# Performance work log

Hardware: AMD Instinct MI355X
Metric: run time of the kernel (lower is better)

## Reference

```python
import jax, jax.numpy as jnp
import numpy as np

B = 1024
IN_Q = 2048
IN_KV = 2048
NH = 16
D = 64
INNER = NH * D
TF = 4
NC = 2
EPS = 1e-5
SLOPE = 0.01  # LeakyReLU default negative slope


def setup_inputs() -> dict:
    key = jax.random.key(0)
    ks = jax.random.split(key, 8)
    s = 0.02
    return {
        "q_input": jax.random.normal(ks[0], (B, IN_Q), jnp.float32),
        "kv_input": jax.random.normal(ks[1], (B, IN_KV), jnp.float32),
        "Wq": jax.random.normal(ks[2], (INNER, IN_Q), jnp.float32) * s,
        "bq": jax.random.normal(ks[3], (INNER,), jnp.float32) * s,
        "Wkv": jax.random.normal(ks[4], (2 * INNER, IN_KV), jnp.float32) * s,
        "bkv": jax.random.normal(ks[5], (2 * INNER,), jnp.float32) * s,
        "bn_w": jnp.ones((TF,), jnp.float32),
        "bn_b": jnp.zeros((TF,), jnp.float32),
        "Wo": jax.random.normal(ks[6], (NC, TF), jnp.float32) * s,
        "bo": jax.random.normal(ks[7], (NC,), jnp.float32) * s,
    }


def reference(q_input, kv_input, Wq, bq, Wkv, bkv, bn_w, bn_b, Wo, bo):
    b = q_input.shape[0]
    # projections: [B, NH, D] and [B, NH, 2D]
    q = (q_input @ Wq.T + bq).reshape(b, NH, D)
    kv = (kv_input @ Wkv.T + bkv).reshape(b, NH, 2 * D)
    k, v = kv[..., :D], kv[..., D:]
    # sim[b,n] = k[b,n,:] . q[b,n,:]  (per-head scalar score)
    sim = jnp.einsum("bnd,bnd->bn", k, q)
    att = jax.nn.softmax(sim, axis=-1)  # softmax over heads
    # torch.matmul([B,NH], [B,NH,D]) broadcast -> out[i,j,:] = sum_n att[j,n] v[i,n,:]
    att_out = jnp.einsum("jn,ind->ijd", att, v)  # [B, B, D]
    flat = att_out.reshape(b, b * D)  # [B, B*D]
    # AdaptiveAvgPool1d to TF bins (L % TF == 0 -> exact reshape-mean)
    pooled = flat.reshape(b, TF, (b * D) // TF).mean(axis=-1)  # [B, TF]
    x = jnp.where(pooled >= 0, pooled, SLOPE * pooled)  # LeakyReLU
    # BatchNorm1d, train mode (batch stats, biased variance)
    mean = x.mean(axis=0)
    var = x.var(axis=0)
    x = (x - mean) * jax.lax.rsqrt(var + EPS) * bn_w + bn_b
    # dropout(p=0.0) is identity
    return x @ Wo.T + bo  # [B, NC]
```

## Files before the change

kernel.cpp:

```cpp
#include <hip/hip_runtime.h>
#include <hip/hip_bf16.h>

#define EPS 1e-5f
#define SLOPE 0.01f

typedef __attribute__((ext_vector_type(8))) short bfrag8;
typedef __attribute__((ext_vector_type(4))) float f32x4;

#define AS1 __attribute__((address_space(1)))
#define AS3 __attribute__((address_space(3)))

#define WS_SIM_OFF   0u
#define WS_S_OFF     65536u
#define WS_WVS_OFF   131072u
#define WS_BVS_OFF   262144u
#define WS_AIMG_OFF  262208u
#define WS_BIMG_OFF  8650816u

__device__ __forceinline__ unsigned short f2bf(float f) {
    union { float f; unsigned int u; } x; x.f = f;
    unsigned int r = (x.u + 0x7FFFu + ((x.u >> 16) & 1u)) >> 16;
    return (unsigned short)r;
}
__device__ __forceinline__ uint4 pack8(const float4& a, const float4& b) {
    uint4 r;
    r.x = (unsigned)f2bf(a.x) | ((unsigned)f2bf(a.y) << 16);
    r.y = (unsigned)f2bf(a.z) | ((unsigned)f2bf(a.w) << 16);
    r.z = (unsigned)f2bf(b.x) | ((unsigned)f2bf(b.y) << 16);
    r.w = (unsigned)f2bf(b.z) | ((unsigned)f2bf(b.w) << 16);
    return r;
}

#define PREP_A    524288
#define PREP_B2   (PREP_A + 524288)
#define PREP_WVSE (PREP_B2 + 32768)
#define PREP_SIMZ (PREP_WVSE + 16384)
#define PREP_END  (PREP_SIMZ + 16)

__global__ __launch_bounds__(256) void prep_kernel(
        const float* __restrict__ qin, const float* __restrict__ kvin,
        const float* __restrict__ Wq, const float* __restrict__ Wkv,
        const float* __restrict__ bkv, unsigned char* __restrict__ ws) {
    int gid = blockIdx.x * 256 + threadIdx.x;
    if (gid < PREP_A) {
        int p  = gid & 511;
        int kt = (gid >> 9) & 31;
        int mt = (gid >> 14) & 15;
        int s2 = gid >> 18;
        int rit = p >> 3;
        int gk = (p & 7) ^ (rit & 7);
        int row = mt * 64 + rit;
        int k = kt * 64 + gk * 8;
        const float* src = (s2 ? kvin : qin) + (size_t)row * 2048 + k;
        float4 v0 = *(const float4*)src;
        float4 v1 = *(const float4*)(src + 4);
        *(uint4*)(ws + WS_AIMG_OFF + (size_t)gid * 16) = pack8(v0, v1);
    } else if (gid < PREP_B2) {
        int g2 = gid - PREP_A;
        int p  = g2 & 511;
        int kt = (g2 >> 9) & 31;
        int dh = (g2 >> 14) & 1;
        int h  = g2 >> 15;
        int cit = p >> 3;
        int gk = (p & 7) ^ (cit & 7);
        int k = kt * 64 + gk * 8;
        const float* wrow;
        if (cit < 32) wrow = Wq  + (size_t)(h * 64 + dh * 32 + cit) * 2048;
        else          wrow = Wkv + (size_t)(h * 128 + dh * 32 + (cit - 32)) * 2048;
        float4 v0 = *(const float4*)(wrow + k);
        float4 v1 = *(const float4*)(wrow + k + 4);
        *(uint4*)(ws + WS_BIMG_OFF + (size_t)g2 * 16) = pack8(v0, v1);
    } else if (gid < PREP_WVSE) {
        int g2 = gid - PREP_B2;
        int n = g2 >> 11, c = g2 & 2047;
        const float* base = Wkv + (size_t)(n * 128 + 64) * 2048 + c;
        float s = 0.f;
        #pragma unroll 8
        for (int d = 0; d < 64; ++d) s += base[(size_t)d * 2048];
        ((float*)(ws + WS_WVS_OFF))[c * 16 + n] = s;
    } else if (gid < PREP_SIMZ) {
        ((float*)(ws + WS_SIM_OFF))[gid - PREP_WVSE] = 0.f;
    } else if (gid < PREP_END) {
        int n = gid - PREP_SIMZ;
        float b = 0.f;
        #pragma unroll
        for (int d = 0; d < 64; ++d) b += bkv[n * 128 + 64 + d];
        ((float*)(ws + WS_BVS_OFF))[n] = b;
    }
}

__global__ __launch_bounds__(256, 2) void gemm_sim_kernel(unsigned char* __restrict__ ws,
        const float* __restrict__ bq, const float* __restrict__ bkv) {
    __shared__ alignas(16) unsigned short LAq[3][4096];
    __shared__ alignas(16) unsigned short LAkv[3][4096];
    __shared__ alignas(16) unsigned short LB[3][4096];

    const int t = threadIdx.x;
    const int w = t >> 6, l = t & 63;
    const int hd = blockIdx.x, mt = blockIdx.y;
    const int h = hd >> 1, dh = hd & 1;
    const int qk = w >> 1, wr = w & 1;
    const int lrow = l & 15, lhi = l >> 4;
    const int m0 = mt * 64;

    const unsigned char* aqBase = ws + WS_AIMG_OFF + (size_t)mt * 262144u;
    const unsigned char* akBase = aqBase + 4194304u;
    const unsigned char* bBase  = ws + WS_BIMG_OFF + (size_t)hd * 262144u;
    float* sim = (float*)(ws + WS_SIM_OFF);

    int offA[2][2], offB[2][2];
    #pragma unroll
    for (int ks = 0; ks < 2; ++ks)
        #pragma unroll
        for (int i = 0; i < 2; ++i) {
            int r = wr * 32 + i * 16 + lrow;
            int c = qk * 32 + i * 16 + lrow;
            offA[ks][i] = r * 128 + (((ks * 4 + lhi) ^ (r & 7)) << 4);
            offB[ks][i] = c * 128 + (((ks * 4 + lhi) ^ (c & 7)) << 4);
        }

    f32x4 acc00 = (f32x4)0.f, acc01 = (f32x4)0.f, acc10 = (f32x4)0.f, acc11 = (f32x4)0.f;

#define STAGE(kt_, buf_) do {                                                        \
    const unsigned char* _aq = aqBase + (size_t)(kt_) * 8192;                        \
    const unsigned char* _ak = akBase + (size_t)(kt_) * 8192;                        \
    const unsigned char* _b  = bBase  + (size_t)(kt_) * 8192;                        \
    unsigned char* _dq = ((unsigned char*)&LAq[0][0])  + (size_t)(buf_) * 8192;      \
    unsigned char* _dk = ((unsigned char*)&LAkv[0][0]) + (size_t)(buf_) * 8192;      \
    unsigned char* _db = ((unsigned char*)&LB[0][0])   + (size_t)(buf_) * 8192;      \
    _Pragma("unroll")                                                                \
    for (int _j = 0; _j < 2; ++_j) {                                                 \
        int _p = _j * 256 + t;                                                       \
        __builtin_amdgcn_global_load_lds(                                            \
            (const AS1 unsigned int*)(const void*)(_aq + _p * 16),                   \
            (AS3 unsigned int*)(void*)(_dq + _p * 16), 16, 0, 0);                    \
        __builtin_amdgcn_global_load_lds(                                            \
            (const AS1 unsigned int*)(const void*)(_ak + _p * 16),                   \
            (AS3 unsigned int*)(void*)(_dk + _p * 16), 16, 0, 0);                    \
        __builtin_amdgcn_global_load_lds(                                            \
            (const AS1 unsigned int*)(const void*)(_b + _p * 16),                    \
            (AS3 unsigned int*)(void*)(_db + _p * 16), 16, 0, 0);                    \
    } } while (0)

    STAGE(0, 0);
    STAGE(1, 1);
    asm volatile("s_waitcnt vmcnt(6)" ::: "memory");
    __builtin_amdgcn_sched_barrier(0);
    __builtin_amdgcn_s_barrier();
    __builtin_amdgcn_sched_barrier(0);

    int cur = 0, nxt = 2;
    for (int kt = 0; kt < 32; ++kt) {
        {
            const char* Ab = (const char*)(qk ? &LAkv[0][0] : &LAq[0][0]) + cur * 8192;
            const char* Bb = (const char*)&LB[0][0] + cur * 8192;
            #pragma unroll
            for (int ks = 0; ks < 2; ++ks) {
                bfrag8 fa0 = *(const bfrag8*)(Ab + offA[ks][0]);
                bfrag8 fa1 = *(const bfrag8*)(Ab + offA[ks][1]);
                bfrag8 fb0 = *(const bfrag8*)(Bb + offB[ks][0]);
                bfrag8 fb1 = *(const bfrag8*)(Bb + offB[ks][1]);
                acc00 = __builtin_amdgcn_mfma_f32_16x16x32_bf16(fa0, fb0, acc00, 0, 0, 0);
                acc01 = __builtin_amdgcn_mfma_f32_16x16x32_bf16(fa0, fb1, acc01, 0, 0, 0);
                acc10 = __builtin_amdgcn_mfma_f32_16x16x32_bf16(fa1, fb0, acc10, 0, 0, 0);
                acc11 = __builtin_amdgcn_mfma_f32_16x16x32_bf16(fa1, fb1, acc11, 0, 0, 0);
            }
        }
        if (kt < 30) {
            STAGE(kt + 2, nxt);
            asm volatile("s_waitcnt vmcnt(6)" ::: "memory");
        } else {
            asm volatile("s_waitcnt vmcnt(0)" ::: "memory");
        }
        __builtin_amdgcn_sched_barrier(0);
        __builtin_amdgcn_s_barrier();
        __builtin_amdgcn_sched_barrier(0);
        cur = (cur == 2) ? 0 : cur + 1;
        nxt = (nxt == 2) ? 0 : nxt + 1;
    }
#undef STAGE

    f32x4 acc[2][2] = {{acc00, acc01}, {acc10, acc11}};
    float biasv[2];
    #pragma unroll
    for (int ni = 0; ni < 2; ++ni) {
        int d = dh * 32 + ni * 16 + lrow;
        biasv[ni] = qk ? bkv[h * 128 + d] : bq[h * 64 + d];
    }
    #pragma unroll
    for (int mi = 0; mi < 2; ++mi)
        #pragma unroll
        for (int ni = 0; ni < 2; ++ni)
            #pragma unroll
            for (int r = 0; r < 4; ++r)
                acc[mi][ni][r] += biasv[ni];

    float (*Cq)[32] = (float(*)[32])&LAq[0][0];
    if (!qk) {
        #pragma unroll
        for (int mi = 0; mi < 2; ++mi)
            #pragma unroll
            for (int ni = 0; ni < 2; ++ni)
                #pragma unroll
                for (int r = 0; r < 4; ++r)
                    Cq[wr * 32 + mi * 16 + lhi * 4 + r][ni * 16 + lrow] = acc[mi][ni][r];
    }
    __syncthreads();
    if (qk) {
        #pragma unroll
        for (int mi = 0; mi < 2; ++mi) {
            float pv[4];
            #pragma unroll
            for (int r = 0; r < 4; ++r) {
                int row = wr * 32 + mi * 16 + lhi * 4 + r;
                pv[r] = Cq[row][lrow]      * acc[mi][0][r]
                      + Cq[row][16 + lrow] * acc[mi][1][r];
            }
            #pragma unroll
            for (int r = 0; r < 4; ++r) {
                float v = pv[r];
                v += __shfl_xor(v, 1); v += __shfl_xor(v, 2);
                v += __shfl_xor(v, 4); v += __shfl_xor(v, 8);
                if ((l & 15) == 0) {
                    int row = wr * 32 + mi * 16 + (l >> 4) * 4 + r;
                    atomicAdd(&sim[(m0 + row) * 16 + h], v);
                }
            }
        }
    }
}

__global__ __launch_bounds__(256) void s_kernel(
        const float* __restrict__ kvin, unsigned char* __restrict__ ws) {
    int b = blockIdx.x, t = threadIdx.x;
    int w = t >> 6, l = t & 63;
    __shared__ float SW[4][16];
    int n = t & 15, g = t >> 4;
    const float* kvrow = kvin + (size_t)b * 2048;
    const float* wv = (const float*)(ws + WS_WVS_OFF);
    float p = 0.f;
    #pragma unroll 4
    for (int tt = 0; tt < 128; ++tt) {
        int c = g + (tt << 4);
        p = fmaf(kvrow[c], wv[c * 16 + n], p);
    }
    p += __shfl_xor(p, 16);
    p += __shfl_xor(p, 32);
    if (l < 16) SW[w][n] = p;
    __syncthreads();
    if (t < 16) {
        float sv = SW[0][t] + SW[1][t] + SW[2][t] + SW[3][t]
                 + ((const float*)(ws + WS_BVS_OFF))[t];
        ((float*)(ws + WS_S_OFF))[b * 16 + t] = sv;
    }
}

__global__ __launch_bounds__(1024) void final_kernel(
        const float* __restrict__ bn_w, const float* __restrict__ bn_b,
        const float* __restrict__ Wo, const float* __restrict__ bo,
        const unsigned char* __restrict__ ws, float* __restrict__ out) {
    int t = threadIdx.x;
    int w = t >> 6;
    int l = t & 63;
    __shared__ float Aw[16][16];
    __shared__ float Af[4][16];
    __shared__ float SWs[16][8];
    __shared__ float FS[8];
    __shared__ float sc[4], sh[4];

    float a16[16];
    {
        const float* srow = (const float*)(ws + WS_SIM_OFF) + (size_t)t * 16;
        float4 v0 = *(const float4*)(srow + 0);
        float4 v1 = *(const float4*)(srow + 4);
        float4 v2 = *(const float4*)(srow + 8);
        float4 v3 = *(const float4*)(srow + 12);
        a16[0]=v0.x; a16[1]=v0.y; a16[2]=v0.z; a16[3]=v0.w;
        a16[4]=v1.x; a16[5]=v1.y; a16[6]=v1.z; a16[7]=v1.w;
        a16[8]=v2.x; a16[9]=v2.y; a16[10]=v2.z; a16[11]=v2.w;
        a16[12]=v3.x; a16[13]=v3.y; a16[14]=v3.z; a16[15]=v3.w;
        float m = a16[0];
        #pragma unroll
        for (int n = 1; n < 16; ++n) m = fmaxf(m, a16[n]);
        float den = 0.f;
        #pragma unroll
        for (int n = 0; n < 16; ++n) { a16[n] = expf(a16[n] - m); den += a16[n]; }
        float inv = 1.f / den;
        #pragma unroll
        for (int n = 0; n < 16; ++n) a16[n] *= inv;
    }
    #pragma unroll
    for (int n = 0; n < 16; ++n) {
        float p = a16[n];
        p += __shfl_xor(p, 1);  p += __shfl_xor(p, 2);
        p += __shfl_xor(p, 4);  p += __shfl_xor(p, 8);
        p += __shfl_xor(p, 16); p += __shfl_xor(p, 32);
        a16[n] = p;
    }
    if (l == 0) {
        #pragma unroll
        for (int n = 0; n < 16; ++n) Aw[w][n] = a16[n];
    }
    __syncthreads();
    if (t < 64) {
        int f = t >> 4, n = t & 15;
        Af[f][n] = Aw[4*f][n] + Aw[4*f+1][n] + Aw[4*f+2][n] + Aw[4*f+3][n];
    }
    __syncthreads();

    float sv[16];
    {
        const float* srow = (const float*)(ws + WS_S_OFF) + (size_t)t * 16;
        float4 v0 = *(const float4*)(srow + 0);
        float4 v1 = *(const float4*)(srow + 4);
        float4 v2 = *(const float4*)(srow + 8);
        float4 v3 = *(const float4*)(srow + 12);
        sv[0]=v0.x; sv[1]=v0.y; sv[2]=v0.z; sv[3]=v0.w;
        sv[4]=v1.x; sv[5]=v1.y; sv[6]=v1.z; sv[7]=v1.w;
        sv[8]=v2.x; sv[9]=v2.y; sv[10]=v2.z; sv[11]=v2.w;
        sv[12]=v3.x; sv[13]=v3.y; sv[14]=v3.z; sv[15]=v3.w;
    }
    float x[4];
    #pragma unroll
    for (int f = 0; f < 4; ++f) {
        float p = 0.f;
        #pragma unroll
        for (int n = 0; n < 16; ++n) p = fmaf(Af[f][n], sv[n], p);
        p *= (1.f / 16384.f);
        x[f] = (p >= 0.f) ? p : SLOPE * p;
    }

    float st[8];
    #pragma unroll
    for (int f = 0; f < 4; ++f) { st[f] = x[f]; st[4 + f] = x[f] * x[f]; }
    #pragma unroll
    for (int j = 0; j < 8; ++j) {
        float p = st[j];
        p += __shfl_xor(p, 1);  p += __shfl_xor(p, 2);
        p += __shfl_xor(p, 4);  p += __shfl_xor(p, 8);
        p += __shfl_xor(p, 16); p += __shfl_xor(p, 32);
        st[j] = p;
    }
    if (l == 0) {
        #pragma unroll
        for (int j = 0; j < 8; ++j) SWs[w][j] = st[j];
    }
    __syncthreads();
    if (t < 8) {
        float p = 0.f;
        #pragma unroll
        for (int ww = 0; ww < 16; ++ww) p += SWs[ww][t];
        FS[t] = p;
    }
    __syncthreads();
    if (t < 4) {
        float mean = FS[t] * (1.f / 1024.f);
        float var  = FS[4 + t] * (1.f / 1024.f) - mean * mean;
        float s = bn_w[t] / sqrtf(var + EPS);
        sc[t] = s;
        sh[t] = bn_b[t] - mean * s;
    }
    __syncthreads();

    float o0 = bo[0], o1 = bo[1];
    #pragma unroll
    for (int f = 0; f < 4; ++f) {
        float xh = x[f] * sc[f] + sh[f];
        o0 = fmaf(xh, Wo[f], o0);
        o1 = fmaf(xh, Wo[4 + f], o1);
    }
    *(float2*)(out + (size_t)t * 2) = make_float2(o0, o1);
}

extern "C" void kernel_launch(void* const* d_in, const int* in_sizes, int n_in,
                              void* d_out, int out_size, void* d_ws, size_t ws_size,
                              hipStream_t stream) {
    const float* q_input  = (const float*)d_in[0];
    const float* kv_input = (const float*)d_in[1];
    const float* Wq   = (const float*)d_in[2];
    const float* bq   = (const float*)d_in[3];
    const float* Wkv  = (const float*)d_in[4];
    const float* bkv  = (const float*)d_in[5];
    const float* bn_w = (const float*)d_in[6];
    const float* bn_b = (const float*)d_in[7];
    const float* Wo   = (const float*)d_in[8];
    const float* bo   = (const float*)d_in[9];
    float* out = (float*)d_out;
    unsigned char* ws = (unsigned char*)d_ws;

    hipLaunchKernelGGL(prep_kernel, dim3((PREP_END + 255) / 256), dim3(256), 0, stream,
                       q_input, kv_input, Wq, Wkv, bkv, ws);
    hipLaunchKernelGGL(gemm_sim_kernel, dim3(32, 16), dim3(256), 0, stream,
                       ws, bq, bkv);
    hipLaunchKernelGGL(s_kernel, dim3(1024), dim3(256), 0, stream, kv_input, ws);
    hipLaunchKernelGGL(final_kernel, dim3(1), dim3(1024), 0, stream,
                       bn_w, bn_b, Wo, bo, ws, out);
}
```

Measured before the change: 60.56 us.

## Process two heads per block in sim GEMM to share staged A tiles

The projection/similarity GEMM block now has 512 threads covering two heads (and one half of D) instead of 256 threads covering one head-half. Both heads share the same Q and KV activation tiles staged in LDS, so each activation tile is loaded from global memory once per pair of heads instead of once per head. The grid shrinks to 8x16x2 blocks at one block per CU with a larger LDS footprint. The trade-off is fewer resident blocks per CU, which may reduce latency hiding.

```diff
diff --git a/kernel.cpp b/kernel.cpp
--- a/kernel.cpp
+++ b/kernel.cpp
@@ -89,23 +89,24 @@
     }
 }
 
-__global__ __launch_bounds__(256, 2) void gemm_sim_kernel(unsigned char* __restrict__ ws,
+__global__ __launch_bounds__(512, 1) void gemm_sim_kernel(unsigned char* __restrict__ ws,
         const float* __restrict__ bq, const float* __restrict__ bkv) {
     __shared__ alignas(16) unsigned short LAq[3][4096];
     __shared__ alignas(16) unsigned short LAkv[3][4096];
-    __shared__ alignas(16) unsigned short LB[3][4096];
+    __shared__ alignas(16) unsigned short LB[3][2][4096];
 
     const int t = threadIdx.x;
     const int w = t >> 6, l = t & 63;
-    const int hd = blockIdx.x, mt = blockIdx.y;
-    const int h = hd >> 1, dh = hd & 1;
-    const int qk = w >> 1, wr = w & 1;
+    const int hp = blockIdx.x, mt = blockIdx.y, dh = blockIdx.z;
+    const int qk = w >> 2, hh = (w >> 1) & 1, wr = w & 1;
+    const int h = hp * 2 + hh;
     const int lrow = l & 15, lhi = l >> 4;
     const int m0 = mt * 64;
 
     const unsigned char* aqBase = ws + WS_AIMG_OFF + (size_t)mt * 262144u;
     const unsigned char* akBase = aqBase + 4194304u;
-    const unsigned char* bBase  = ws + WS_BIMG_OFF + (size_t)hd * 262144u;
+    const unsigned char* bBase0 = ws + WS_BIMG_OFF + (size_t)((hp * 2 + 0) * 2 + dh) * 262144u;
+    const unsigned char* bBase1 = ws + WS_BIMG_OFF + (size_t)((hp * 2 + 1) * 2 + dh) * 262144u;
     float* sim = (float*)(ws + WS_SIM_OFF);
 
     int offA[2][2], offB[2][2];
@@ -122,29 +123,27 @@
     f32x4 acc00 = (f32x4)0.f, acc01 = (f32x4)0.f, acc10 = (f32x4)0.f, acc11 = (f32x4)0.f;
 
 #define STAGE(kt_, buf_) do {                                                        \
-    const unsigned char* _aq = aqBase + (size_t)(kt_) * 8192;                        \
-    const unsigned char* _ak = akBase + (size_t)(kt_) * 8192;                        \
-    const unsigned char* _b  = bBase  + (size_t)(kt_) * 8192;                        \
-    unsigned char* _dq = ((unsigned char*)&LAq[0][0])  + (size_t)(buf_) * 8192;      \
-    unsigned char* _dk = ((unsigned char*)&LAkv[0][0]) + (size_t)(buf_) * 8192;      \
-    unsigned char* _db = ((unsigned char*)&LB[0][0])   + (size_t)(buf_) * 8192;      \
-    _Pragma("unroll")                                                                \
-    for (int _j = 0; _j < 2; ++_j) {                                                 \
-        int _p = _j * 256 + t;                                                       \
-        __builtin_amdgcn_global_load_lds(                                            \
-            (const AS1 unsigned int*)(const void*)(_aq + _p * 16),                   \
-            (AS3 unsigned int*)(void*)(_dq + _p * 16), 16, 0, 0);                    \
-        __builtin_amdgcn_global_load_lds(                                            \
-            (const AS1 unsigned int*)(const void*)(_ak + _p * 16),                   \
-            (AS3 unsigned int*)(void*)(_dk + _p * 16), 16, 0, 0);                    \
-        __builtin_amdgcn_global_load_lds(                                            \
-            (const AS1 unsigned int*)(const void*)(_b + _p * 16),                    \
-            (AS3 unsigned int*)(void*)(_db + _p * 16), 16, 0, 0);                    \
-    } } while (0)
+    const unsigned char* _aq = aqBase + (size_t)(kt_) * 8192 + t * 16;               \
+    const unsigned char* _ak = akBase + (size_t)(kt_) * 8192 + t * 16;               \
+    const unsigned char* _b0 = bBase0 + (size_t)(kt_) * 8192 + t * 16;               \
+    const unsigned char* _b1 = bBase1 + (size_t)(kt_) * 8192 + t * 16;               \
+    unsigned char* _dq = ((unsigned char*)&LAq[0][0])  + (size_t)(buf_) * 8192 + t * 16;  \
+    unsigned char* _dk = ((unsigned char*)&LAkv[0][0]) + (size_t)(buf_) * 8192 + t * 16;  \
+    unsigned char* _d0 = ((unsigned char*)&LB[0][0][0]) + (size_t)(buf_) * 16384 + t * 16;        \
+    unsigned char* _d1 = ((unsigned char*)&LB[0][0][0]) + (size_t)(buf_) * 16384 + 8192 + t * 16; \
+    __builtin_amdgcn_global_load_lds((const AS1 unsigned int*)(const void*)_aq,      \
+        (AS3 unsigned int*)(void*)_dq, 16, 0, 0);                                    \
+    __builtin_amdgcn_global_load_lds((const AS1 unsigned int*)(const void*)_ak,      \
+        (AS3 unsigned int*)(void*)_dk, 16, 0, 0);                                    \
+    __builtin_amdgcn_global_load_lds((const AS1 unsigned int*)(const void*)_b0,      \
+        (AS3 unsigned int*)(void*)_d0, 16, 0, 0);                                    \
+    __builtin_amdgcn_global_load_lds((const AS1 unsigned int*)(const void*)_b1,      \
+        (AS3 unsigned int*)(void*)_d1, 16, 0, 0);                                    \
+    } while (0)
 
     STAGE(0, 0);
     STAGE(1, 1);
-    asm volatile("s_waitcnt vmcnt(6)" ::: "memory");
+    asm volatile("s_waitcnt vmcnt(4)" ::: "memory");
     __builtin_amdgcn_sched_barrier(0);
     __builtin_amdgcn_s_barrier();
     __builtin_amdgcn_sched_barrier(0);
@@ -153,7 +152,7 @@
     for (int kt = 0; kt < 32; ++kt) {
         {
             const char* Ab = (const char*)(qk ? &LAkv[0][0] : &LAq[0][0]) + cur * 8192;
-            const char* Bb = (const char*)&LB[0][0] + cur * 8192;
+            const char* Bb = (const char*)&LB[0][0][0] + cur * 16384 + hh * 8192;
             #pragma unroll
             for (int ks = 0; ks < 2; ++ks) {
                 bfrag8 fa0 = *(const bfrag8*)(Ab + offA[ks][0]);
@@ -168,7 +167,7 @@
         }
         if (kt < 30) {
             STAGE(kt + 2, nxt);
-            asm volatile("s_waitcnt vmcnt(6)" ::: "memory");
+            asm volatile("s_waitcnt vmcnt(4)" ::: "memory");
         } else {
             asm volatile("s_waitcnt vmcnt(0)" ::: "memory");
         }
@@ -195,15 +194,17 @@
             for (int r = 0; r < 4; ++r)
                 acc[mi][ni][r] += biasv[ni];
 
-    float (*Cq)[32] = (float(*)[32])&LAq[0][0];
+    float* cqs = (float*)&LAq[0][0];
     if (!qk) {
         #pragma unroll
         for (int mi = 0; mi < 2; ++mi)
             #pragma unroll
             for (int ni = 0; ni < 2; ++ni)
                 #pragma unroll
-                for (int r = 0; r < 4; ++r)
-                    Cq[wr * 32 + mi * 16 + lhi * 4 + r][ni * 16 + lrow] = acc[mi][ni][r];
+                for (int r = 0; r < 4; ++r) {
+                    int row = mi * 16 + lhi * 4 + r;
+                    cqs[(((hh * 2 + wr) * 32 + row) * 32) + ni * 16 + lrow] = acc[mi][ni][r];
+                }
     }
     __syncthreads();
     if (qk) {
@@ -212,9 +213,9 @@
             float pv[4];
             #pragma unroll
             for (int r = 0; r < 4; ++r) {
-                int row = wr * 32 + mi * 16 + lhi * 4 + r;
-                pv[r] = Cq[row][lrow]      * acc[mi][0][r]
-                      + Cq[row][16 + lrow] * acc[mi][1][r];
+                int row = mi * 16 + lhi * 4 + r;
+                const float* crow = cqs + ((hh * 2 + wr) * 32 + row) * 32;
+                pv[r] = crow[lrow] * acc[mi][0][r] + crow[16 + lrow] * acc[mi][1][r];
             }
             #pragma unroll
             for (int r = 0; r < 4; ++r) {
@@ -390,7 +391,7 @@
 
     hipLaunchKernelGGL(prep_kernel, dim3((PREP_END + 255) / 256), dim3(256), 0, stream,
                        q_input, kv_input, Wq, Wkv, bkv, ws);
-    hipLaunchKernelGGL(gemm_sim_kernel, dim3(32, 16), dim3(256), 0, stream,
+    hipLaunchKernelGGL(gemm_sim_kernel, dim3(8, 16, 2), dim3(512), 0, stream,
                        ws, bq, bkv);
     hipLaunchKernelGGL(s_kernel, dim3(1024), dim3(256), 0, stream, kv_input, ws);
     hipLaunchKernelGGL(final_kernel, dim3(1), dim3(1024), 0, stream,
```

Result: no change. 59.74 us, median of 3 (-1.4%).
